# Kernel tuning notes

Hardware: AMD Instinct MI355X
Metric: run time of the kernel (lower is better)

The kernel has to match this reference:

```python
import jax, jax.numpy as jnp
import numpy as np

B, T, C = 2, 2048, 1024
N_HEAD = 16
HEAD_DIM = C // N_HEAD


def setup_inputs() -> dict:
    key = jax.random.key(0)
    ks = jax.random.split(key, 5)
    s = 0.02
    return {
        "x": jax.random.normal(ks[0], (B, T, C), dtype=jnp.float32),
        "W_kqv": jax.random.normal(ks[1], (C, 3 * C), dtype=jnp.float32) * s,
        "b_kqv": jax.random.normal(ks[2], (3 * C,), dtype=jnp.float32) * s,
        "W_proj": jax.random.normal(ks[3], (C, C), dtype=jnp.float32) * s,
        "b_proj": jax.random.normal(ks[4], (C,), dtype=jnp.float32) * s,
    }


def reference(x, W_kqv, b_kqv, W_proj, b_proj):
    Bx, Tx, Cx = x.shape
    qkv = x @ W_kqv + b_kqv                      # [B, T, 3C]
    q, k, v = jnp.split(qkv, 3, axis=-1)
    # [B, H, T, D]
    q = q.reshape(Bx, Tx, N_HEAD, HEAD_DIM).transpose(0, 2, 1, 3)
    k = k.reshape(Bx, Tx, N_HEAD, HEAD_DIM).transpose(0, 2, 1, 3)
    v = v.reshape(Bx, Tx, N_HEAD, HEAD_DIM).transpose(0, 2, 1, 3)
    scale = 1.0 / jnp.sqrt(jnp.asarray(HEAD_DIM, dtype=x.dtype))
    att = jnp.einsum("bhqd,bhkd->bhqk", q, k) * scale  # [B, H, T, T]
    causal = jnp.tril(jnp.ones((Tx, Tx), dtype=bool))   # [T, T]
    att = jnp.where(causal[None, None], att, jnp.float32(-jnp.inf))
    att = jax.nn.softmax(att, axis=-1)
    y = jnp.einsum("bhqk,bhkd->bhqd", att, v)            # [B, H, T, D]
    y = y.transpose(0, 2, 1, 3).reshape(Bx, Tx, Cx)
    out = y @ W_proj + b_proj
    return out, k, v
```

## Files before the change

kernel.cpp:

```cpp
#include <hip/hip_runtime.h>


#define DEVI __device__ __forceinline__

typedef unsigned short ushort_t;
typedef unsigned long long u64_t;
typedef __attribute__((ext_vector_type(4))) unsigned short us4;
typedef __attribute__((ext_vector_type(8))) unsigned short ushort8;
typedef __attribute__((ext_vector_type(4))) float f32x4;
typedef __attribute__((ext_vector_type(8))) __bf16 bf16x8;

DEVI unsigned short f2bf(float f) {
  union { float f; unsigned int u; } c; c.f = f;
  unsigned int u = c.u;
  unsigned int r = (u + 0x7FFFu + ((u >> 16) & 1u)) >> 16;
  return (unsigned short)r;
}

DEVI float exp2v(float x) {
  float r;
  asm("v_exp_f32 %0, %1\n\ts_nop 0" : "=v"(r) : "v"(x));
  return r;
}

DEVI unsigned int cvtpk(float lo, float hi) {
  unsigned int r;
  asm("v_cvt_pk_bf16_f32 %0, %1, %2" : "=v"(r) : "v"(lo), "v"(hi));
  return r;
}

DEVI f32x4 mfma16(ushort8 a, ushort8 b, f32x4 c) {
  return __builtin_amdgcn_mfma_f32_16x16x32_bf16(
      __builtin_bit_cast(bf16x8, a), __builtin_bit_cast(bf16x8, b), c, 0, 0, 0);
}

typedef const __attribute__((address_space(1))) void* gptr_t;
typedef __attribute__((address_space(3))) void* lptr_t;
#define GLOAD_LDS16(g, l) \
  __builtin_amdgcn_global_load_lds((gptr_t)(g), (lptr_t)(l), 16, 0, 0)

DEVI void bar() {
  asm volatile("" ::: "memory");
  __builtin_amdgcn_s_barrier();
  asm volatile("" ::: "memory");
}
#define VMCNT(n) asm volatile("s_waitcnt vmcnt(" #n ")" ::: "memory")


__global__ void prep_kernel(const float* __restrict__ x,
                            const float* __restrict__ Wk,
                            const float* __restrict__ Wp,
                            ushort_t* __restrict__ Xb,
                            ushort_t* __restrict__ Wkt,
                            ushort_t* __restrict__ Wpt) {
  __shared__ float tile[32][33];
  const int id = blockIdx.x, tid = threadIdx.x;
  if (id < 2048) {
    const int i = id * 256 + tid;
    const f32x4* p = (const f32x4*)x;
    f32x4 a = p[2 * i], b = p[2 * i + 1];
    ushort8 o;
    o[0] = f2bf(a[0]); o[1] = f2bf(a[1]); o[2] = f2bf(a[2]); o[3] = f2bf(a[3]);
    o[4] = f2bf(b[0]); o[5] = f2bf(b[1]); o[6] = f2bf(b[2]); o[7] = f2bf(b[3]);
    ((ushort8*)Xb)[i] = o;
    return;
  }
  const float* in;
  ushort_t* outp;
  int R = 1024, Cin, bx, by;
  if (id < 5120) {
    const int jid = id - 2048;
    bx = jid % 96; by = jid / 96; in = Wk; outp = Wkt; Cin = 3072;
  } else {
    const int jid = id - 5120;
    bx = jid % 32; by = jid / 32; in = Wp; outp = Wpt; Cin = 1024;
  }
  const int c0 = bx * 32, r0 = by * 32;
  const int tx = tid & 31, ty = tid >> 5;
#pragma unroll
  for (int it = 0; it < 4; ++it)
    tile[ty + it * 8][tx] = in[(size_t)(r0 + ty + it * 8) * Cin + c0 + tx];
  __syncthreads();
#pragma unroll
  for (int it = 0; it < 4; ++it)
    outp[(size_t)(c0 + ty + it * 8) * R + r0 + tx] = f2bf(tile[tx][ty + it * 8]);
}


__global__ __launch_bounds__(256) void gemm_bt_kernel(
    const ushort_t* __restrict__ A, const ushort_t* __restrict__ Bt,
    const float* __restrict__ bias, float* __restrict__ outF,
    float* __restrict__ outK, float* __restrict__ outV,
    ushort_t* __restrict__ Qb, ushort_t* __restrict__ Kb, ushort_t* __restrict__ Vb,
    int M, int N, int K, int mode) {
  __shared__ __align__(16) ushort_t As[128 * 64];
  __shared__ __align__(16) ushort_t Bs[128 * 64];
  const int tid = threadIdx.x;
  const int w = tid >> 6, lane = tid & 63;
  const int wr = w >> 1, wc = w & 1;
  const int nby = gridDim.y;
  const int chy = nby >> 3;
  const int orig = blockIdx.x + gridDim.x * blockIdx.y;
  const int xcd = orig & 7, idx = orig >> 3;
  const int by = xcd * chy + (idx % chy);
  const int bx = idx / chy;
  const int m0 = by * 128, n0 = bx * 128;
  const int l15 = lane & 15, lhi = lane >> 4;
  const int rowA = lane >> 3;
  const int sgc = (((lane & 7) ^ ((lane >> 3) & 7)) << 3);

  f32x4 acc[4][4] = {};

  const int nk = K >> 6;
  for (int kt = 0; kt < nk; ++kt) {
    const size_t k0 = (size_t)kt << 6;
    if (kt) bar();
#pragma unroll
    for (int it = 0; it < 4; ++it) {
      const int rbase = (w * 4 + it) * 8;
      GLOAD_LDS16(A + (size_t)(m0 + rbase + rowA) * K + k0 + sgc, &As[rbase * 64]);
      GLOAD_LDS16(Bt + (size_t)(n0 + rbase + rowA) * K + k0 + sgc, &Bs[rbase * 64]);
    }
    VMCNT(0);
    bar();
#pragma unroll
    for (int kk = 0; kk < 2; ++kk) {
      const int gof = (((kk * 4 + lhi) ^ (l15 & 7)) << 3);
      ushort8 a[4], b[4];
#pragma unroll
      for (int i = 0; i < 4; ++i)
        a[i] = *(const ushort8*)&As[(wr * 64 + i * 16 + l15) * 64 + gof];
#pragma unroll
      for (int j = 0; j < 4; ++j)
        b[j] = *(const ushort8*)&Bs[(wc * 64 + j * 16 + l15) * 64 + gof];
#pragma unroll
      for (int i = 0; i < 4; ++i)
#pragma unroll
        for (int j = 0; j < 4; ++j) acc[i][j] = mfma16(a[i], b[j], acc[i][j]);
    }
  }

  const float QSCALE = 0.18033688011112042f;
#pragma unroll
  for (int i = 0; i < 4; ++i) {
#pragma unroll
    for (int j = 0; j < 4; ++j) {
      const int nn = n0 + wc * 64 + j * 16 + l15;
      const float bv = bias[nn];
#pragma unroll
      for (int r = 0; r < 4; ++r) {
        const int mm = m0 + wr * 64 + i * 16 + lhi * 4 + r;
        const float v = acc[i][j][r] + bv;
        if (mode == 0) {
          outF[(size_t)mm * N + nn] = v;
        } else {
          const int bb = mm >> 11, t = mm & 2047;
          const int c = nn & 1023, h = c >> 6, d = c & 63;
          const size_t idx2 = ((size_t)(bb * 16 + h) * 2048 + t) * 64 + d;
          const int sec = nn >> 10;
          if (sec == 0) {
            Qb[idx2] = f2bf(v * QSCALE);
          } else if (sec == 1) {
            outK[idx2] = v; Kb[idx2] = f2bf(v);
          } else {
            outV[idx2] = v; Vb[idx2] = f2bf(v);
          }
        }
      }
    }
  }
}


__global__ __launch_bounds__(256) void gemm_bt64_kernel(
    const ushort_t* __restrict__ A, const ushort_t* __restrict__ Bt,
    const float* __restrict__ bias, float* __restrict__ outF,
    int M, int N, int K) {
  __shared__ __align__(16) ushort_t As[64 * 64];
  __shared__ __align__(16) ushort_t Bs[128 * 64];
  const int tid = threadIdx.x;
  const int w = tid >> 6, lane = tid & 63;
  const int wr = w >> 1, wc = w & 1;
  const int nby = gridDim.y;
  const int chy = nby >> 3;
  const int orig = blockIdx.x + gridDim.x * blockIdx.y;
  const int xcd = orig & 7, idx = orig >> 3;
  const int by = xcd * chy + (idx % chy);
  const int bx = idx / chy;
  const int m0 = by * 64, n0 = bx * 128;
  const int l15 = lane & 15, lhi = lane >> 4;
  const int rowA = lane >> 3;
  const int sgc = (((lane & 7) ^ ((lane >> 3) & 7)) << 3);

  f32x4 acc[2][4] = {};

  const int nk = K >> 6;
  for (int kt = 0; kt < nk; ++kt) {
    const size_t k0 = (size_t)kt << 6;
    if (kt) bar();
#pragma unroll
    for (int it = 0; it < 2; ++it) {
      const int rbase = (w * 2 + it) * 8;
      GLOAD_LDS16(A + (size_t)(m0 + rbase + rowA) * K + k0 + sgc, &As[rbase * 64]);
    }
#pragma unroll
    for (int it = 0; it < 4; ++it) {
      const int rbase = (w * 4 + it) * 8;
      GLOAD_LDS16(Bt + (size_t)(n0 + rbase + rowA) * K + k0 + sgc, &Bs[rbase * 64]);
    }
    VMCNT(0);
    bar();
#pragma unroll
    for (int kk = 0; kk < 2; ++kk) {
      const int gof = (((kk * 4 + lhi) ^ (l15 & 7)) << 3);
      ushort8 a[2], b[4];
#pragma unroll
      for (int i = 0; i < 2; ++i)
        a[i] = *(const ushort8*)&As[(wr * 32 + i * 16 + l15) * 64 + gof];
#pragma unroll
      for (int j = 0; j < 4; ++j)
        b[j] = *(const ushort8*)&Bs[(wc * 64 + j * 16 + l15) * 64 + gof];
#pragma unroll
      for (int i = 0; i < 2; ++i)
#pragma unroll
        for (int j = 0; j < 4; ++j) acc[i][j] = mfma16(a[i], b[j], acc[i][j]);
    }
  }

#pragma unroll
  for (int i = 0; i < 2; ++i) {
#pragma unroll
    for (int j = 0; j < 4; ++j) {
      const int nn = n0 + wc * 64 + j * 16 + l15;
      const float bv = bias[nn];
#pragma unroll
      for (int r = 0; r < 4; ++r) {
        const int mm = m0 + wr * 32 + i * 16 + lhi * 4 + r;
        outF[(size_t)mm * N + nn] = acc[i][j][r] + bv;
      }
    }
  }
}


__global__ __launch_bounds__(512) void attn_kernel(
    const ushort_t* __restrict__ Qb, const ushort_t* __restrict__ Kb,
    const ushort_t* __restrict__ Vb, ushort_t* __restrict__ Yb) {
  __shared__ __align__(16) ushort_t Ks[2][64 * 64];
  __shared__ __align__(16) ushort_t Vt[2][64 * 72];
  __shared__ __align__(16) ushort_t Pl[8 * 16 * 72];
  const int id = blockIdx.x;
  const int xcd = id & 7;
  int qt, bh;
  if (id < 256) {
    const int j = id >> 3;
    bh = xcd + 8 * (j & 3);
    qt = 8 + (j >> 2);
  } else {
    const int j = (id - 256) >> 3;
    bh = xcd + 8 * (j & 3);
    qt = 7 - (j >> 2);
  }
  const int b = bh >> 4, h = bh & 15;
  const int tid = threadIdx.x, w = tid >> 6, lane = tid & 63;
  const int l15 = lane & 15, lhi = lane >> 4;
  const int swzP = 2 * (l15 & 3);
  const size_t base = (size_t)bh * 2048 * 64;
  const float NEG_INF = -__builtin_inff();
  ushort_t* myP = &Pl[w * 16 * 72];

  const int krow = tid >> 3, kg = tid & 7;
  const int ksg = kg ^ (krow & 7);
  const int vd0 = (tid & 15) * 4;
  const int vt0 = (tid >> 4) * 2;

  const int nkt = 2 * qt + 2;
  const int qrow = w * 16 + l15;

  ushort8 qf[2];
  {
    const size_t qrg = base + (size_t)(qt * 128 + qrow) * 64;
    qf[0] = *(const ushort8*)&Qb[qrg + lhi * 8];
    qf[1] = *(const ushort8*)&Qb[qrg + 32 + lhi * 8];
  }
  float m_s = NEG_INF, l_s = 0.f;
  f32x4 o[4] = {};

  {
    GLOAD_LDS16(Kb + base + (size_t)krow * 64 + ksg * 8, &Ks[0][tid * 8]);
    const ushort_t* vp = Vb + base + (size_t)vt0 * 64 + vd0;
    u64_t a = *(const u64_t*)vp;
    u64_t c = *(const u64_t*)(vp + 64);
    us4 av = __builtin_bit_cast(us4, a);
    us4 cv = __builtin_bit_cast(us4, c);
#pragma unroll
    for (int i = 0; i < 4; ++i) {
      const int d = vd0 + i;
      const int scg = (vt0 >> 3) ^ ((d >> 3) & 7);
      unsigned int wv = (unsigned int)av[i] | ((unsigned int)cv[i] << 16);
      *(unsigned int*)&Vt[0][d * 72 + scg * 8 + (vt0 & 7)] = wv;
    }
  }
  __syncthreads();

  for (int kt = 0; kt < nkt; ++kt) {
    const int cur = kt & 1, nxt = cur ^ 1;
    const bool pf = (kt + 1 < nkt);
    u64_t va = 0, vc = 0;
    if (pf) {
      const size_t tb = base + (size_t)(kt + 1) * 64 * 64;
      GLOAD_LDS16(Kb + tb + (size_t)krow * 64 + ksg * 8, &Ks[nxt][tid * 8]);
      const ushort_t* vp = Vb + tb + (size_t)vt0 * 64 + vd0;
      va = *(const u64_t*)vp;
      vc = *(const u64_t*)(vp + 64);
    }

    f32x4 s[4] = {};
#pragma unroll
    for (int kk = 0; kk < 2; ++kk) {
#pragma unroll
      for (int j = 0; j < 4; ++j) {
        const int g = (kk * 4 + lhi) ^ (l15 & 7);
        ushort8 kb = *(const ushort8*)&Ks[cur][(j * 16 + l15) * 64 + g * 8];
        s[j] = mfma16(kb, qf[kk], s[j]);
      }
    }
    if (64 * kt + 63 > 128 * qt + w * 16) {
      const int delta = 128 * qt + qrow - 64 * kt;
#pragma unroll
      for (int j = 0; j < 4; ++j)
#pragma unroll
        for (int r = 0; r < 4; ++r)
          if ((j * 16 + lhi * 4 + r) > delta) s[j][r] = NEG_INF;
    }

    float pmax = s[0][0];
#pragma unroll
    for (int j = 0; j < 4; ++j)
#pragma unroll
      for (int r = 0; r < 4; ++r) pmax = fmaxf(pmax, s[j][r]);
    pmax = fmaxf(pmax, __shfl_xor(pmax, 16));
    pmax = fmaxf(pmax, __shfl_xor(pmax, 32));
    if (__any(pmax - m_s > 8.0f)) {
      const float mnew = fmaxf(m_s, pmax);
      const float al = exp2v(m_s - mnew);
      m_s = mnew;
      l_s *= al;
#pragma unroll
      for (int df = 0; df < 4; ++df)
#pragma unroll
        for (int r = 0; r < 4; ++r) o[df][r] *= al;
    }
    float rsum = 0.f;
#pragma unroll
    for (int j = 0; j < 4; ++j)
#pragma unroll
      for (int r = 0; r < 4; ++r) {
        const float pe = exp2v(s[j][r] - m_s);
        s[j][r] = pe;
        rsum += pe;
      }
    rsum += __shfl_xor(rsum, 16);
    rsum += __shfl_xor(rsum, 32);
    l_s += rsum;

#pragma unroll
    for (int j = 0; j < 4; ++j) {
      const unsigned int w0 = cvtpk(s[j][0], s[j][1]);
      const unsigned int w1 = cvtpk(s[j][2], s[j][3]);
      const u64_t dw = (u64_t)w0 | ((u64_t)w1 << 32);
      const int cg = j * 2 + (lhi >> 1);
      *(u64_t*)&myP[l15 * 72 + ((cg ^ swzP) << 3) + ((lhi & 1) << 2)] = dw;
    }

#pragma unroll
    for (int kk = 0; kk < 2; ++kk) {
      ushort8 pa = *(const ushort8*)&myP[l15 * 72 + (((kk * 4 + lhi) ^ swzP) << 3)];
#pragma unroll
      for (int df = 0; df < 4; ++df) {
        const int r = df * 16 + l15;
        const int g = (kk * 4 + lhi) ^ ((r >> 3) & 7);
        ushort8 vb = *(const ushort8*)&Vt[cur][r * 72 + g * 8];
        o[df] = mfma16(vb, pa, o[df]);
      }
    }

    if (pf) {
      us4 av = __builtin_bit_cast(us4, va);
      us4 cv = __builtin_bit_cast(us4, vc);
#pragma unroll
      for (int i = 0; i < 4; ++i) {
        const int d = vd0 + i;
        const int scg = (vt0 >> 3) ^ ((d >> 3) & 7);
        unsigned int wv = (unsigned int)av[i] | ((unsigned int)cv[i] << 16);
        *(unsigned int*)&Vt[nxt][d * 72 + scg * 8 + (vt0 & 7)] = wv;
      }
    }
    __syncthreads();
  }

  const float inv = 1.0f / l_s;
  const size_t yrow = (size_t)(b * 2048 + qt * 128 + qrow) * 1024 + h * 64;
#pragma unroll
  for (int df = 0; df < 4; ++df) {
    us4 ov;
#pragma unroll
    for (int r = 0; r < 4; ++r) ov[r] = f2bf(o[df][r] * inv);
    *(us4*)&Yb[yrow + df * 16 + lhi * 4] = ov;
  }
}


extern "C" void kernel_launch(void* const* d_in, const int* in_sizes, int n_in,
                              void* d_out, int out_size, void* d_ws, size_t ws_size,
                              hipStream_t stream) {
  const float* x      = (const float*)d_in[0];
  const float* W_kqv  = (const float*)d_in[1];
  const float* b_kqv  = (const float*)d_in[2];
  const float* W_proj = (const float*)d_in[3];
  const float* b_proj = (const float*)d_in[4];
  float* out  = (float*)d_out;
  float* outK = out + 4194304;
  float* outV = out + 8388608;

  char* ws = (char*)d_ws;
  ushort_t* Xb  = (ushort_t*)(ws);
  ushort_t* Wkt = (ushort_t*)(ws + ((size_t)8 << 20));
  ushort_t* Wpt = (ushort_t*)(ws + ((size_t)14 << 20));
  ushort_t* Qb  = (ushort_t*)(ws + ((size_t)16 << 20));
  ushort_t* Kb  = (ushort_t*)(ws + ((size_t)24 << 20));
  ushort_t* Vb  = (ushort_t*)(ws + ((size_t)32 << 20));
  ushort_t* Yb  = Xb;

  prep_kernel<<<6144, 256, 0, stream>>>(x, W_kqv, W_proj, Xb, Wkt, Wpt);
  gemm_bt_kernel<<<dim3(24, 32), 256, 0, stream>>>(
      Xb, Wkt, b_kqv, nullptr, outK, outV, Qb, Kb, Vb, 4096, 3072, 1024, 1);
  attn_kernel<<<512, 512, 0, stream>>>(Qb, Kb, Vb, Yb);
  gemm_bt64_kernel<<<dim3(8, 64), 256, 0, stream>>>(
      Yb, Wpt, b_proj, out, 4096, 1024, 1024);
}
```

Before: 106.7 us.

## Split attention into 64-row query tiles with single-buffered K/V loads

The attention kernel now handles 64 query rows per block with 4 waves (256 threads) instead of 128 rows with 8 waves, doubling the grid to 1024 blocks. The grid order is reworked so heavy and light causal tiles interleave across generations. K/V double-buffering and register prefetch are dropped: each iteration loads the tile, waits on vmcnt/lgkmcnt and synchronizes before computing. The aim is better load balance and occupancy from smaller LDS use, at the cost of exposed load latency and each K/V tile being fetched by twice as many blocks.

After: 109.3 us. 2.5% more time.

```diff
diff --git a/kernel.cpp b/kernel.cpp
--- a/kernel.cpp
+++ b/kernel.cpp
@@ -45,6 +45,7 @@
   asm volatile("" ::: "memory");
 }
 #define VMCNT(n) asm volatile("s_waitcnt vmcnt(" #n ")" ::: "memory")
+#define LGKM0 asm volatile("s_waitcnt lgkmcnt(0)" ::: "memory")
 
 
 __global__ void prep_kernel(const float* __restrict__ x,
@@ -243,24 +244,21 @@
 }
 
 
-__global__ __launch_bounds__(512) void attn_kernel(
+__global__ __launch_bounds__(256) void attn_kernel(
     const ushort_t* __restrict__ Qb, const ushort_t* __restrict__ Kb,
     const ushort_t* __restrict__ Vb, ushort_t* __restrict__ Yb) {
-  __shared__ __align__(16) ushort_t Ks[2][64 * 64];
-  __shared__ __align__(16) ushort_t Vt[2][64 * 72];
-  __shared__ __align__(16) ushort_t Pl[8 * 16 * 72];
+  __shared__ __align__(16) ushort_t Ks[64 * 64];
+  __shared__ __align__(16) ushort_t Vt[64 * 72];
+  __shared__ __align__(16) ushort_t Pl[4 * 16 * 72];
   const int id = blockIdx.x;
-  const int xcd = id & 7;
-  int qt, bh;
-  if (id < 256) {
-    const int j = id >> 3;
-    bh = xcd + 8 * (j & 3);
-    qt = 8 + (j >> 2);
-  } else {
-    const int j = (id - 256) >> 3;
-    bh = xcd + 8 * (j & 3);
-    qt = 7 - (j >> 2);
-  }
+  const int xcd = id & 7, win = id >> 3;
+  const int gen = win >> 5, jj = (win >> 2) & 7;
+  const int bh = xcd + 8 * (win & 3);
+  int qt;
+  if (gen == 0) qt = 31 - jj;
+  else if (gen == 1) qt = 16 + jj;
+  else if (gen == 2) qt = 15 - jj;
+  else qt = jj;
   const int b = bh >> 4, h = bh & 15;
   const int tid = threadIdx.x, w = tid >> 6, lane = tid & 63;
   const int l15 = lane & 15, lhi = lane >> 4;
@@ -269,51 +267,49 @@
   const float NEG_INF = -__builtin_inff();
   ushort_t* myP = &Pl[w * 16 * 72];
 
-  const int krow = tid >> 3, kg = tid & 7;
-  const int ksg = kg ^ (krow & 7);
   const int vd0 = (tid & 15) * 4;
-  const int vt0 = (tid >> 4) * 2;
-
-  const int nkt = 2 * qt + 2;
-  const int qrow = w * 16 + l15;
+  const int vt0b = (tid >> 4) * 2;
+
+  const int nkt = qt + 1;
 
   ushort8 qf[2];
   {
-    const size_t qrg = base + (size_t)(qt * 128 + qrow) * 64;
-    qf[0] = *(const ushort8*)&Qb[qrg + lhi * 8];
-    qf[1] = *(const ushort8*)&Qb[qrg + 32 + lhi * 8];
+    const size_t qrow = base + (size_t)(qt * 64 + w * 16 + l15) * 64;
+    qf[0] = *(const ushort8*)&Qb[qrow + lhi * 8];
+    qf[1] = *(const ushort8*)&Qb[qrow + 32 + lhi * 8];
   }
   float m_s = NEG_INF, l_s = 0.f;
   f32x4 o[4] = {};
 
-  {
-    GLOAD_LDS16(Kb + base + (size_t)krow * 64 + ksg * 8, &Ks[0][tid * 8]);
-    const ushort_t* vp = Vb + base + (size_t)vt0 * 64 + vd0;
-    u64_t a = *(const u64_t*)vp;
-    u64_t c = *(const u64_t*)(vp + 64);
-    us4 av = __builtin_bit_cast(us4, a);
-    us4 cv = __builtin_bit_cast(us4, c);
-#pragma unroll
-    for (int i = 0; i < 4; ++i) {
-      const int d = vd0 + i;
-      const int scg = (vt0 >> 3) ^ ((d >> 3) & 7);
-      unsigned int wv = (unsigned int)av[i] | ((unsigned int)cv[i] << 16);
-      *(unsigned int*)&Vt[0][d * 72 + scg * 8 + (vt0 & 7)] = wv;
-    }
-  }
-  __syncthreads();
-
   for (int kt = 0; kt < nkt; ++kt) {
-    const int cur = kt & 1, nxt = cur ^ 1;
-    const bool pf = (kt + 1 < nkt);
-    u64_t va = 0, vc = 0;
-    if (pf) {
-      const size_t tb = base + (size_t)(kt + 1) * 64 * 64;
-      GLOAD_LDS16(Kb + tb + (size_t)krow * 64 + ksg * 8, &Ks[nxt][tid * 8]);
-      const ushort_t* vp = Vb + tb + (size_t)vt0 * 64 + vd0;
-      va = *(const u64_t*)vp;
-      vc = *(const u64_t*)(vp + 64);
-    }
+    if (kt) bar();
+    const size_t tb = base + (size_t)kt * 4096;
+#pragma unroll
+    for (int it = 0; it < 2; ++it) {
+      const int chunk = tid + it * 256;
+      const int row = chunk >> 3, g = chunk & 7;
+      const int sg = g ^ (row & 7);
+      GLOAD_LDS16(Kb + tb + (size_t)row * 64 + sg * 8, &Ks[chunk * 8]);
+    }
+#pragma unroll
+    for (int it = 0; it < 2; ++it) {
+      const int t0 = vt0b + it * 32;
+      const ushort_t* vp = Vb + tb + (size_t)t0 * 64 + vd0;
+      u64_t a = *(const u64_t*)vp;
+      u64_t c = *(const u64_t*)(vp + 64);
+      us4 av = __builtin_bit_cast(us4, a);
+      us4 cv = __builtin_bit_cast(us4, c);
+#pragma unroll
+      for (int i = 0; i < 4; ++i) {
+        const int d = vd0 + i;
+        const int scg = (t0 >> 3) ^ ((d >> 3) & 7);
+        unsigned int wv = (unsigned int)av[i] | ((unsigned int)cv[i] << 16);
+        *(unsigned int*)&Vt[d * 72 + scg * 8 + (t0 & 7)] = wv;
+      }
+    }
+    VMCNT(0);
+    LGKM0;
+    bar();
 
     f32x4 s[4] = {};
 #pragma unroll
@@ -321,17 +317,17 @@
 #pragma unroll
       for (int j = 0; j < 4; ++j) {
         const int g = (kk * 4 + lhi) ^ (l15 & 7);
-        ushort8 kb = *(const ushort8*)&Ks[cur][(j * 16 + l15) * 64 + g * 8];
+        ushort8 kb = *(const ushort8*)&Ks[(j * 16 + l15) * 64 + g * 8];
         s[j] = mfma16(kb, qf[kk], s[j]);
       }
     }
-    if (64 * kt + 63 > 128 * qt + w * 16) {
-      const int delta = 128 * qt + qrow - 64 * kt;
+    const int qloc = w * 16 + l15;
+    if (kt == qt) {
 #pragma unroll
       for (int j = 0; j < 4; ++j)
 #pragma unroll
         for (int r = 0; r < 4; ++r)
-          if ((j * 16 + lhi * 4 + r) > delta) s[j][r] = NEG_INF;
+          if ((j * 16 + lhi * 4 + r) > qloc) s[j][r] = NEG_INF;
     }
 
     float pmax = s[0][0];
@@ -380,27 +376,14 @@
       for (int df = 0; df < 4; ++df) {
         const int r = df * 16 + l15;
         const int g = (kk * 4 + lhi) ^ ((r >> 3) & 7);
-        ushort8 vb = *(const ushort8*)&Vt[cur][r * 72 + g * 8];
+        ushort8 vb = *(const ushort8*)&Vt[r * 72 + g * 8];
         o[df] = mfma16(vb, pa, o[df]);
       }
     }
-
-    if (pf) {
-      us4 av = __builtin_bit_cast(us4, va);
-      us4 cv = __builtin_bit_cast(us4, vc);
-#pragma unroll
-      for (int i = 0; i < 4; ++i) {
-        const int d = vd0 + i;
-        const int scg = (vt0 >> 3) ^ ((d >> 3) & 7);
-        unsigned int wv = (unsigned int)av[i] | ((unsigned int)cv[i] << 16);
-        *(unsigned int*)&Vt[nxt][d * 72 + scg * 8 + (vt0 & 7)] = wv;
-      }
-    }
-    __syncthreads();
   }
 
   const float inv = 1.0f / l_s;
-  const size_t yrow = (size_t)(b * 2048 + qt * 128 + qrow) * 1024 + h * 64;
+  const size_t yrow = (size_t)(b * 2048 + qt * 64 + w * 16 + l15) * 1024 + h * 64;
 #pragma unroll
   for (int df = 0; df < 4; ++df) {
     us4 ov;
@@ -435,7 +418,7 @@
   prep_kernel<<<6144, 256, 0, stream>>>(x, W_kqv, W_proj, Xb, Wkt, Wpt);
   gemm_bt_kernel<<<dim3(24, 32), 256, 0, stream>>>(
       Xb, Wkt, b_kqv, nullptr, outK, outV, Qb, Kb, Vb, 4096, 3072, 1024, 1);
-  attn_kernel<<<512, 512, 0, stream>>>(Qb, Kb, Vb, Yb);
+  attn_kernel<<<1024, 256, 0, stream>>>(Qb, Kb, Vb, Yb);
   gemm_bt64_kernel<<<dim3(8, 64), 256, 0, stream>>>(
       Yb, Wpt, b_proj, out, 4096, 1024, 1024);
 }
```
